# Optimization experiments

Measured on AMD Instinct MI355X. Metric: run time of the kernel, lower is better.

The kernel has to match this reference:

```python
import jax, jax.numpy as jnp
import numpy as np

U_NUM, I_NUM, EMBED, NUM_LAYERS = 100000, 50000, 64, 3
N_NODES = U_NUM + I_NUM
BATCH = 8192


def _build_laplacian(rng):
    # Faithful to buildLaplacianMat: symmetric bipartite rating matrix with
    # D^-1/2 A D^-1/2 normalization (degree = count of nonzeros per row).
    nnz = 2_000_000
    u = rng.integers(0, U_NUM, nnz)
    i = rng.integers(0, I_NUM, nnz)
    lin = np.unique(u.astype(np.int64) * I_NUM + i)  # dedupe (user,item) pairs
    u = (lin // I_NUM).astype(np.int32)
    i = (lin % I_NUM).astype(np.int32)
    rating = rng.integers(1, 6, u.shape[0]).astype(np.float32)
    rows = np.concatenate([u, i + U_NUM])
    cols = np.concatenate([i + U_NUM, u])
    vals = np.concatenate([rating, rating])
    deg = np.bincount(rows, minlength=N_NODES)
    dinv = np.where(deg > 0, deg.astype(np.float64) ** -0.5, 0.0).astype(np.float32)
    vals = dinv[rows] * vals * dinv[cols]
    return rows, cols, vals


def setup_inputs() -> dict:
    key = jax.random.key(0)
    k1, k2 = jax.random.split(key)
    rng = np.random.default_rng(0)
    rows, cols, vals = _build_laplacian(rng)
    # xavier_uniform over [num, embed]: bound = sqrt(6/(fan_in+fan_out))
    bu = float(np.sqrt(6.0 / (U_NUM + EMBED)))
    bi = float(np.sqrt(6.0 / (I_NUM + EMBED)))
    uEmbd = jax.random.uniform(k1, (U_NUM, EMBED), jnp.float32, -bu, bu)
    iEmbd = jax.random.uniform(k2, (I_NUM, EMBED), jnp.float32, -bi, bi)
    userIdx = jnp.asarray(rng.integers(0, U_NUM, BATCH), dtype=jnp.int64)
    itemIdx = jnp.asarray(rng.integers(0, I_NUM, BATCH), dtype=jnp.int64)
    return {
        "uEmbd": uEmbd,
        "iEmbd": iEmbd,
        "lap_rows": jnp.asarray(rows, jnp.int32),
        "lap_cols": jnp.asarray(cols, jnp.int32),
        "lap_vals": jnp.asarray(vals, jnp.float32),
        "userIdx": userIdx,
        "itemIdx": itemIdx,
    }


def _spmm(rows, cols, vals, x):
    # sparse [N,N] @ dense [N,D] via edge-list gather + segment-sum
    return jax.ops.segment_sum(vals[:, None] * x[cols], rows, num_segments=N_NODES)


def reference(uEmbd, iEmbd, lap_rows, lap_cols, lap_vals, userIdx, itemIdx):
    feats = jnp.concatenate([uEmbd, iEmbd], axis=0)  # [N, D]
    acc = feats
    f = feats
    for _ in range(NUM_LAYERS):
        f = _spmm(lap_rows, lap_cols, lap_vals, f)
        acc = acc + f
    final = acc / (NUM_LAYERS + 1)  # mean over stacked layer embeddings
    ue = final[userIdx]                      # [B, D]
    ie = final[itemIdx + U_NUM]              # [B, D]
    return jnp.sum(ue * ie, axis=1)          # [B]
```

## Files before the change

kernel.cpp:

```cpp
#include <hip/hip_runtime.h>

#define U_NUMC 100000
#define I_NUMC 50000
#define NNODES 150000
#define EMB 64
#define NBATCH 8192
#define NB_I ((I_NUMC + 255) / 256)

__global__ __launch_bounds__(256) void k_init(const float* __restrict__ uE,
                                              const float* __restrict__ iE,
                                              float* __restrict__ f0,
                                              float* __restrict__ acc) {
    const int total = NNODES * EMB / 4;
    const int uCount = U_NUMC * EMB / 4;
    const float4* u4 = (const float4*)uE;
    const float4* i4 = (const float4*)iE;
    for (int idx = blockIdx.x * blockDim.x + threadIdx.x; idx < total;
         idx += gridDim.x * blockDim.x) {
        float4 v = (idx < uCount) ? u4[idx] : i4[idx - uCount];
        ((float4*)f0)[idx] = v;
        ((float4*)acc)[idx] = v;
    }
}

__global__ __launch_bounds__(256) void k_zero(int* __restrict__ p, int n) {
    int i = blockIdx.x * blockDim.x + threadIdx.x;
    if (i < n) p[i] = 0;
}

__global__ __launch_bounds__(256) void k_uptr(const int* __restrict__ rows1, int E1,
                                              int* __restrict__ uptr) {
    int r = blockIdx.x * blockDim.x + threadIdx.x;
    if (r > U_NUMC) return;
    int lo = 0, hi = E1;
    while (lo < hi) {
        int mid = (lo + hi) >> 1;
        if (rows1[mid] < r) lo = mid + 1; else hi = mid;
    }
    uptr[r] = lo;
}

__global__ __launch_bounds__(256) void k_hist(const int* __restrict__ cols1, int E1,
                                              int* __restrict__ hist) {
    int e = blockIdx.x * blockDim.x + threadIdx.x;
    if (e >= E1) return;
    atomicAdd(&hist[cols1[e] - U_NUMC], 1);
}

__global__ __launch_bounds__(256) void k_scan1(const int* __restrict__ hist,
                                               int* __restrict__ bsum) {
    int b = blockIdx.x, t = threadIdx.x;
    int idx = b * 256 + t;
    int v = (idx < I_NUMC) ? hist[idx] : 0;
    #pragma unroll
    for (int o = 32; o; o >>= 1) v += __shfl_xor(v, o);
    __shared__ int ws4[4];
    if ((t & 63) == 0) ws4[t >> 6] = v;
    __syncthreads();
    if (t == 0) bsum[b] = ws4[0] + ws4[1] + ws4[2] + ws4[3];
}

__global__ __launch_bounds__(256) void k_scan2(const int* __restrict__ bsum,
                                               int* __restrict__ boff,
                                               int* __restrict__ iptr) {
    __shared__ int lds[256];
    int t = threadIdx.x;
    int v = (t < NB_I) ? bsum[t] : 0;
    int x = v;
    #pragma unroll
    for (int o = 1; o < 256; o <<= 1) {
        lds[t] = x; __syncthreads();
        int y = (t >= o) ? lds[t - o] : 0; __syncthreads();
        x += y;
    }
    if (t < NB_I) boff[t] = x - v;
    if (t == 255) iptr[I_NUMC] = x;
}

__global__ __launch_bounds__(256) void k_scan3(const int* __restrict__ hist,
                                               const int* __restrict__ boff,
                                               int* __restrict__ iptr,
                                               int* __restrict__ cursor) {
    __shared__ int lds[256];
    int b = blockIdx.x, t = threadIdx.x;
    int idx = b * 256 + t;
    int v = (idx < I_NUMC) ? hist[idx] : 0;
    int x = v;
    #pragma unroll
    for (int o = 1; o < 256; o <<= 1) {
        lds[t] = x; __syncthreads();
        int y = (t >= o) ? lds[t - o] : 0; __syncthreads();
        x += y;
    }
    if (idx < I_NUMC) {
        int excl = boff[b] + x - v;
        iptr[idx] = excl;
        cursor[idx] = excl;
    }
}

__global__ __launch_bounds__(256) void k_scatter(const int* __restrict__ rows1,
                                                 const int* __restrict__ cols1,
                                                 const float* __restrict__ vals1,
                                                 int E1,
                                                 int* __restrict__ cursor,
                                                 int* __restrict__ item_u,
                                                 float* __restrict__ item_v) {
    int e = blockIdx.x * blockDim.x + threadIdx.x;
    if (e >= E1) return;
    int i = cols1[e] - U_NUMC;
    int pos = atomicAdd(&cursor[i], 1);
    item_u[pos] = rows1[e];
    item_v[pos] = vals1[e];
}

__global__ __launch_bounds__(256) void k_spmm(const float* __restrict__ f,
                                              float* __restrict__ fn,
                                              float* __restrict__ acc,
                                              const int* __restrict__ uptr,
                                              const int* __restrict__ cols1,
                                              const float* __restrict__ vals1,
                                              const int* __restrict__ iptr,
                                              const int* __restrict__ item_u,
                                              const float* __restrict__ item_v) {
    int wave = (blockIdx.x * blockDim.x + threadIdx.x) >> 6;
    int lane = threadIdx.x & 63;
    if (wave >= NNODES) return;

    int beg, end;
    const int* ci;
    const float* vi;
    if (wave < U_NUMC) {
        beg = uptr[wave]; end = uptr[wave + 1];
        ci = cols1; vi = vals1;
    } else {
        int i = wave - U_NUMC;
        beg = iptr[i]; end = iptr[i + 1];
        ci = item_u; vi = item_v;
    }

    float sum = 0.f;
    for (int base = beg; base < end; base += 64) {
        int idx = base + lane;
        int ld = min(idx, end - 1);
        int c = ci[ld];
        float v = (idx < end) ? vi[ld] : 0.f;
        int n = min(64, end - base);
        for (int j = 0; j < n; j += 8) {
            float l[8], vv[8];
            #pragma unroll
            for (int t = 0; t < 8; ++t) {
                int cj = __shfl(c, j + t);
                vv[t] = __shfl(v, j + t);
                l[t] = f[cj * EMB + lane];
            }
            #pragma unroll
            for (int t = 0; t < 8; ++t) sum += vv[t] * l[t];
        }
    }
    int o = wave * EMB + lane;
    fn[o] = sum;
    acc[o] += sum;
}

__global__ __launch_bounds__(256) void k_out(const float* __restrict__ acc,
                                             const int* __restrict__ userIdx,
                                             const int* __restrict__ itemIdx,
                                             float* __restrict__ out) {
    int wave = (blockIdx.x * blockDim.x + threadIdx.x) >> 6;
    int lane = threadIdx.x & 63;
    if (wave >= NBATCH) return;
    int u = userIdx[wave];
    int it = itemIdx[wave] + U_NUMC;
    float p = acc[u * EMB + lane] * acc[it * EMB + lane];
    #pragma unroll
    for (int offd = 32; offd; offd >>= 1) p += __shfl_xor(p, offd);
    if (lane == 0) out[wave] = p * (1.0f / 16.0f);
}

extern "C" void kernel_launch(void* const* d_in, const int* in_sizes, int n_in,
                              void* d_out, int out_size, void* d_ws, size_t ws_size,
                              hipStream_t stream) {
    const float* uE      = (const float*)d_in[0];
    const float* iE      = (const float*)d_in[1];
    const int*   rows    = (const int*)d_in[2];
    const int*   cols    = (const int*)d_in[3];
    const float* vals    = (const float*)d_in[4];
    const int*   userIdx = (const int*)d_in[5];
    const int*   itemIdx = (const int*)d_in[6];
    const int E  = in_sizes[2];
    const int E1 = E / 2;

    char* ws = (char*)d_ws;
    size_t off = 0;
    auto alloc = [&](size_t bytes) -> void* {
        off = (off + 255) & ~(size_t)255;
        void* p = ws + off;
        off += bytes;
        return p;
    };
    float* f0     = (float*)alloc((size_t)NNODES * EMB * 4);
    float* f1     = (float*)alloc((size_t)NNODES * EMB * 4);
    float* acc    = (float*)alloc((size_t)NNODES * EMB * 4);
    int*   uptr   = (int*)alloc((size_t)(U_NUMC + 1) * 4);
    int*   iptr   = (int*)alloc((size_t)(I_NUMC + 1) * 4);
    int*   hist   = (int*)alloc((size_t)I_NUMC * 4);
    int*   cursor = (int*)alloc((size_t)I_NUMC * 4);
    int*   bsum   = (int*)alloc((size_t)NB_I * 4);
    int*   boff   = (int*)alloc((size_t)NB_I * 4);
    int*   item_u = (int*)alloc((size_t)E1 * 4);
    float* item_v = (float*)alloc((size_t)E1 * 4);

    k_init<<<2048, 256, 0, stream>>>(uE, iE, f0, acc);
    k_zero<<<(I_NUMC + 255) / 256, 256, 0, stream>>>(hist, I_NUMC);

    k_uptr<<<(U_NUMC + 256) / 256, 256, 0, stream>>>(rows, E1, uptr);
    k_hist<<<(E1 + 255) / 256, 256, 0, stream>>>(cols, E1, hist);
    k_scan1<<<NB_I, 256, 0, stream>>>(hist, bsum);
    k_scan2<<<1, 256, 0, stream>>>(bsum, boff, iptr);
    k_scan3<<<NB_I, 256, 0, stream>>>(hist, boff, iptr, cursor);
    k_scatter<<<(E1 + 255) / 256, 256, 0, stream>>>(rows, cols, vals, E1,
                                                    cursor, item_u, item_v);

    const int spmm_blocks = NNODES / 4;
    const float* fc = f0;
    float* fn = f1;
    for (int l = 0; l < 3; ++l) {
        k_spmm<<<spmm_blocks, 256, 0, stream>>>(fc, fn, acc,
                                                uptr, cols, vals,
                                                iptr, item_u, item_v);
        float* t = (float*)fc; fc = fn; fn = t;
    }

    k_out<<<NBATCH / 4, 256, 0, stream>>>(acc, userIdx, itemIdx, (float*)d_out);
}
```

Before: 763.9 us.

## Fuse embedding init into first SpMM layer and pack item CSC entries

```diff
diff --git a/kernel.cpp b/kernel.cpp
--- a/kernel.cpp
+++ b/kernel.cpp
@@ -6,22 +6,6 @@
 #define EMB 64
 #define NBATCH 8192
 #define NB_I ((I_NUMC + 255) / 256)
-
-__global__ __launch_bounds__(256) void k_init(const float* __restrict__ uE,
-                                              const float* __restrict__ iE,
-                                              float* __restrict__ f0,
-                                              float* __restrict__ acc) {
-    const int total = NNODES * EMB / 4;
-    const int uCount = U_NUMC * EMB / 4;
-    const float4* u4 = (const float4*)uE;
-    const float4* i4 = (const float4*)iE;
-    for (int idx = blockIdx.x * blockDim.x + threadIdx.x; idx < total;
-         idx += gridDim.x * blockDim.x) {
-        float4 v = (idx < uCount) ? u4[idx] : i4[idx - uCount];
-        ((float4*)f0)[idx] = v;
-        ((float4*)acc)[idx] = v;
-    }
-}
 
 __global__ __launch_bounds__(256) void k_zero(int* __restrict__ p, int n) {
     int i = blockIdx.x * blockDim.x + threadIdx.x;
@@ -104,47 +88,51 @@
                                                  const float* __restrict__ vals1,
                                                  int E1,
                                                  int* __restrict__ cursor,
-                                                 int* __restrict__ item_u,
-                                                 float* __restrict__ item_v) {
+                                                 int2* __restrict__ item_uv) {
     int e = blockIdx.x * blockDim.x + threadIdx.x;
     if (e >= E1) return;
     int i = cols1[e] - U_NUMC;
     int pos = atomicAdd(&cursor[i], 1);
-    item_u[pos] = rows1[e];
-    item_v[pos] = vals1[e];
-}
-
-__global__ __launch_bounds__(256) void k_spmm(const float* __restrict__ f,
+    item_uv[pos] = make_int2(rows1[e], __float_as_int(vals1[e]));
+}
+
+template <int FIRST, int LAST>
+__global__ __launch_bounds__(256) void k_spmm(const float* __restrict__ uE,
+                                              const float* __restrict__ iE,
+                                              const float* __restrict__ f,
                                               float* __restrict__ fn,
                                               float* __restrict__ acc,
                                               const int* __restrict__ uptr,
                                               const int* __restrict__ cols1,
                                               const float* __restrict__ vals1,
                                               const int* __restrict__ iptr,
-                                              const int* __restrict__ item_u,
-                                              const float* __restrict__ item_v) {
+                                              const int2* __restrict__ item_uv) {
     int wave = (blockIdx.x * blockDim.x + threadIdx.x) >> 6;
     int lane = threadIdx.x & 63;
     if (wave >= NNODES) return;
 
+    const bool isUser = (wave < U_NUMC);
     int beg, end;
-    const int* ci;
-    const float* vi;
-    if (wave < U_NUMC) {
-        beg = uptr[wave]; end = uptr[wave + 1];
-        ci = cols1; vi = vals1;
-    } else {
-        int i = wave - U_NUMC;
-        beg = iptr[i]; end = iptr[i + 1];
-        ci = item_u; vi = item_v;
-    }
+    if (isUser) { beg = uptr[wave];           end = uptr[wave + 1]; }
+    else        { int i = wave - U_NUMC; beg = iptr[i]; end = iptr[i + 1]; }
+
+    const float* fb;
+    if (FIRST) fb = isUser ? (iE - (size_t)U_NUMC * EMB) : uE;
+    else       fb = f;
 
     float sum = 0.f;
     for (int base = beg; base < end; base += 64) {
         int idx = base + lane;
         int ld = min(idx, end - 1);
-        int c = ci[ld];
-        float v = (idx < end) ? vi[ld] : 0.f;
+        int c; float v;
+        if (isUser) {
+            c = cols1[ld];
+            v = (idx < end) ? vals1[ld] : 0.f;
+        } else {
+            int2 e = item_uv[ld];
+            c = e.x;
+            v = (idx < end) ? __int_as_float(e.y) : 0.f;
+        }
         int n = min(64, end - base);
         for (int j = 0; j < n; j += 8) {
             float l[8], vv[8];
@@ -152,15 +140,21 @@
             for (int t = 0; t < 8; ++t) {
                 int cj = __shfl(c, j + t);
                 vv[t] = __shfl(v, j + t);
-                l[t] = f[cj * EMB + lane];
+                l[t] = fb[(size_t)cj * EMB + lane];
             }
             #pragma unroll
             for (int t = 0; t < 8; ++t) sum += vv[t] * l[t];
         }
     }
     int o = wave * EMB + lane;
-    fn[o] = sum;
-    acc[o] += sum;
+    if (!LAST) fn[o] = sum;
+    if (FIRST) {
+        float own = isUser ? uE[(size_t)wave * EMB + lane]
+                           : iE[(size_t)(wave - U_NUMC) * EMB + lane];
+        acc[o] = own + sum;
+    } else {
+        acc[o] += sum;
+    }
 }
 
 __global__ __launch_bounds__(256) void k_out(const float* __restrict__ acc,
@@ -199,38 +193,33 @@
         off += bytes;
         return p;
     };
-    float* f0     = (float*)alloc((size_t)NNODES * EMB * 4);
-    float* f1     = (float*)alloc((size_t)NNODES * EMB * 4);
-    float* acc    = (float*)alloc((size_t)NNODES * EMB * 4);
-    int*   uptr   = (int*)alloc((size_t)(U_NUMC + 1) * 4);
-    int*   iptr   = (int*)alloc((size_t)(I_NUMC + 1) * 4);
-    int*   hist   = (int*)alloc((size_t)I_NUMC * 4);
-    int*   cursor = (int*)alloc((size_t)I_NUMC * 4);
-    int*   bsum   = (int*)alloc((size_t)NB_I * 4);
-    int*   boff   = (int*)alloc((size_t)NB_I * 4);
-    int*   item_u = (int*)alloc((size_t)E1 * 4);
-    float* item_v = (float*)alloc((size_t)E1 * 4);
-
-    k_init<<<2048, 256, 0, stream>>>(uE, iE, f0, acc);
+    float* f0      = (float*)alloc((size_t)NNODES * EMB * 4);
+    float* f1      = (float*)alloc((size_t)NNODES * EMB * 4);
+    float* acc     = (float*)alloc((size_t)NNODES * EMB * 4);
+    int*   uptr    = (int*)alloc((size_t)(U_NUMC + 1) * 4);
+    int*   iptr    = (int*)alloc((size_t)(I_NUMC + 1) * 4);
+    int*   hist    = (int*)alloc((size_t)I_NUMC * 4);
+    int*   cursor  = (int*)alloc((size_t)I_NUMC * 4);
+    int*   bsum    = (int*)alloc((size_t)NB_I * 4);
+    int*   boff    = (int*)alloc((size_t)NB_I * 4);
+    int2*  item_uv = (int2*)alloc((size_t)E1 * 8);
+
     k_zero<<<(I_NUMC + 255) / 256, 256, 0, stream>>>(hist, I_NUMC);
-
     k_uptr<<<(U_NUMC + 256) / 256, 256, 0, stream>>>(rows, E1, uptr);
     k_hist<<<(E1 + 255) / 256, 256, 0, stream>>>(cols, E1, hist);
     k_scan1<<<NB_I, 256, 0, stream>>>(hist, bsum);
     k_scan2<<<1, 256, 0, stream>>>(bsum, boff, iptr);
     k_scan3<<<NB_I, 256, 0, stream>>>(hist, boff, iptr, cursor);
     k_scatter<<<(E1 + 255) / 256, 256, 0, stream>>>(rows, cols, vals, E1,
-                                                    cursor, item_u, item_v);
+                                                    cursor, item_uv);
 
     const int spmm_blocks = NNODES / 4;
-    const float* fc = f0;
-    float* fn = f1;
-    for (int l = 0; l < 3; ++l) {
-        k_spmm<<<spmm_blocks, 256, 0, stream>>>(fc, fn, acc,
-                                                uptr, cols, vals,
-                                                iptr, item_u, item_v);
-        float* t = (float*)fc; fc = fn; fn = t;
-    }
+    k_spmm<1, 0><<<spmm_blocks, 256, 0, stream>>>(uE, iE, nullptr, f1, acc,
+                                                  uptr, cols, vals, iptr, item_uv);
+    k_spmm<0, 0><<<spmm_blocks, 256, 0, stream>>>(uE, iE, f1, f0, acc,
+                                                  uptr, cols, vals, iptr, item_uv);
+    k_spmm<0, 1><<<spmm_blocks, 256, 0, stream>>>(uE, iE, f0, nullptr, acc,
+                                                  uptr, cols, vals, iptr, item_uv);
 
     k_out<<<NBATCH / 4, 256, 0, stream>>>(acc, userIdx, itemIdx, (float*)d_out);
 }
```

New measurement: 735.0 us. 3.8% less time.
